# Kernel optimization log

Hardware: AMD Instinct MI355X
Metric: run time of the kernel (lower is better)

## Reference

```python
import jax, jax.numpy as jnp
import numpy as np

B, H, N = 2, 4, 8192
K = 32       # sub_size
TEMP = 2.0   # temperature for the soft permutation indicator


def setup_inputs() -> dict:
    key = jax.random.key(0)
    ranking = jax.random.normal(key, (B, H, N, 1), dtype=jnp.float32)
    return {"ranking": ranking, "i": 0, "j": N}


@jax.custom_vjp
def hsigmoid(x):
    # Hard step indicator (x > 0) with straight-through gradient (CoCN Hsigmoid)
    return (x > 0).astype(x.dtype)

def _hs_fwd(x):
    return hsigmoid(x), None

def _hs_bwd(res, g):
    return (g,)

hsigmoid.defvjp(_hs_fwd, _hs_bwd)


def _windows(x, n, k):
    # circular pad last dim by k-1, then unfold into sliding windows of size k
    xp = jnp.concatenate([x, x[..., :k - 1]], axis=-1)
    idx = jnp.arange(n)[:, None] + jnp.arange(k)[None, :]   # (n, k)
    return xp[..., idx]                                      # (..., n, k)


def reference(ranking, i, j):
    b, h, n = ranking.shape[:3]
    k = K
    r = ranking[..., 0]                                      # (b,h,n)
    order = jnp.argsort(r, axis=2, stable=True)              # (b,h,n) stable sort indices
    r_sorted = jnp.take_along_axis(r, order, axis=2)

    val_win = _windows(r_sorted, n, k)                       # (b,h,n,k)
    idx_win = _windows(order.astype(jnp.float32), n, k).astype(jnp.int32)

    # scatter windows back to original node order == gather by inverse permutation
    inv = jnp.argsort(order, axis=2)                         # (b,h,n)
    val_win = jnp.take_along_axis(val_win, inv[..., None], axis=2)
    idx_win = jnp.take_along_axis(idx_win, inv[..., None], axis=2)

    # within each window, sort by original node index (stable), reorder values alike
    k_order = jnp.argsort(idx_win, axis=-1, stable=True)
    sorted_idx = jnp.take_along_axis(idx_win, k_order, axis=-1)
    val_win = jnp.take_along_axis(val_win, k_order, axis=-1)

    # slice node window [i, i+j)
    val_win = val_win[:, :, i:i + j]                         # (b,h,j,k)
    sorted_idx = sorted_idx[:, :, i:i + j]

    # (b,j,h,k) -> (b*j, h, k, 1)
    x = jnp.transpose(val_win, (0, 2, 1, 3)).reshape(-1, h, k, 1)
    rel = x - jnp.swapaxes(x, -1, -2)                        # (b*j,h,k,k)
    tie_bias = jnp.triu((rel == 0).astype(jnp.float32), 1)   # break ties above diagonal
    rel = rel + tie_bias
    uni = hsigmoid(jax.nn.relu(rel))                         # 1 where strictly greater
    rank = jnp.sum(uni, axis=-2, keepdims=True)              # (b*j,h,1,k)

    ind = jnp.arange(k, dtype=jnp.float32)[:, None] - rank   # (b*j,h,k,k)
    ind = jnp.where(ind < 0, ind + k, ind)
    perm = jnp.exp(-ind * TEMP)
    return perm, sorted_idx
```

## Files before the change

### kernel.cpp

```cpp
#include <hip/hip_runtime.h>
#include <stdint.h>

#define B_ 2
#define H_ 4
#define N_ 8192
#define K_ 32
#define ROWS 8
#define NTOT (ROWS * N_)
#define PERM_ELEMS ((size_t)B_ * N_ * H_ * K_ * K_)

#define JT 1024
#define EPT 8

__device__ __forceinline__ uint32_t mono(float f) {
    uint32_t u = __float_as_uint(f);
    return (u & 0x80000000u) ? ~u : (u | 0x80000000u);
}

__global__ __launch_bounds__(256) void rank_count(const float* __restrict__ ranking,
                                                  int* __restrict__ partial) {
    __shared__ uint64_t jk[JT];
    const int blk = blockIdx.x;
    const int jt  = blk & 7;
    const int it  = (blk >> 3) & 3;
    const int row = blk >> 5;
    const float* rr = ranking + (size_t)row * N_;

    for (int j = threadIdx.x; j < JT; j += 256) {
        const int jj = jt * JT + j;
        jk[j] = ((uint64_t)mono(rr[jj]) << 13) | (uint32_t)jj;
    }

    uint64_t my[EPT];
    const int ibase = it * (EPT * 256) + threadIdx.x;
    #pragma unroll
    for (int e = 0; e < EPT; ++e) {
        const int ii = ibase + e * 256;
        my[e] = ((uint64_t)mono(rr[ii]) << 13) | (uint32_t)ii;
    }
    __syncthreads();

    int cnt[EPT] = {0, 0, 0, 0, 0, 0, 0, 0};
    const ulonglong2* jv = (const ulonglong2*)jk;
    for (int j = 0; j < JT / 2; j += 2) {
        const ulonglong2 a = jv[j];
        const ulonglong2 b = jv[j + 1];
        #pragma unroll
        for (int e = 0; e < EPT; ++e) {
            cnt[e] += (a.x < my[e]);
            cnt[e] += (a.y < my[e]);
            cnt[e] += (b.x < my[e]);
            cnt[e] += (b.y < my[e]);
        }
    }
    #pragma unroll
    for (int e = 0; e < EPT; ++e)
        partial[(size_t)jt * NTOT + (size_t)row * N_ + ibase + e * 256] = cnt[e];
}

__global__ __launch_bounds__(256) void scatter_sorted(const float* __restrict__ ranking,
                                                      const int* __restrict__ partial,
                                                      int2* __restrict__ vid,
                                                      int* __restrict__ inv) {
    const int g = blockIdx.x * 256 + threadIdx.x;
    const int row = g >> 13;
    int s = 0;
    #pragma unroll
    for (int jt = 0; jt < 8; ++jt) s += partial[(size_t)jt * NTOT + g];
    inv[g] = s;
    vid[(size_t)row * N_ + s] = make_int2(__float_as_int(ranking[g]), g & (N_ - 1));
}

__global__ __launch_bounds__(256) void windows_kernel(
    const int2* __restrict__ vid,
    const int* __restrict__ inv,
    float* __restrict__ perm_out,
    float* __restrict__ idx_out)
{
    __shared__ uint64_t wk[8][K_];
    __shared__ float4 cinfo[8][K_];

    const int tid  = threadIdx.x;
    const int wave = tid >> 6;
    const int lane = tid & 63;
    const int half = lane >> 5;
    const int m    = lane & 31;
    const int ws   = wave * 2 + half;

    const int w   = blockIdx.x * 8 + ws;
    const int row = w >> 13;
    const int n   = w & (N_ - 1);

    const int t = inv[(size_t)row * N_ + n];
    int g = t + m; if (g >= N_) g -= N_;
    const int2 vi = vid[(size_t)row * N_ + g];
    const int id = vi.y;
    const int rid = (N_ - 1) - id;
    const uint64_t key2 = ((uint64_t)mono(__int_as_float(vi.x)) << 13) | (uint32_t)rid;

    wk[ws][m] = key2;
    __syncthreads();

    int rank = 0, pos = 0;
    #pragma unroll
    for (int p = 0; p < K_; ++p) {
        const uint64_t kp = wk[ws][p];
        rank += (kp > key2);
        pos  += ((int)((uint32_t)kp & (uint32_t)(N_ - 1)) > rid);
    }

    cinfo[ws][pos] = make_float4(__expf(2.0f * (float)rank),
                                 __int_as_float(rank), (float)id, 0.0f);
    __syncthreads();

    idx_out[((size_t)row * N_ + n) * K_ + m] = cinfo[ws][m].z;

    const int b = row >> 2;
    const int h = row & 3;
    float4* pout = (float4*)(perm_out + (((size_t)b * N_ + n) * H_ + h) * (K_ * K_));

    const int j0 = (m & 7) * 4;
    const float4 c0 = cinfo[ws][j0 + 0];
    const float4 c1 = cinfo[ws][j0 + 1];
    const float4 c2 = cinfo[ws][j0 + 2];
    const float4 c3 = cinfo[ws][j0 + 3];
    const int r0 = __float_as_int(c0.y), r1 = __float_as_int(c1.y);
    const int r2 = __float_as_int(c2.y), r3 = __float_as_int(c3.y);

    const int mbase = m >> 3;
    float a = (mbase & 1 ? 0.13533528f : 1.0f) * (mbase & 2 ? 0.018315639f : 1.0f);
    const float EM8 = 3.3546262e-4f;
    const float E64C = 1.6038108e-28f;
    int mm = mbase;

    #pragma unroll
    for (int q = 0; q < 8; ++q) {
        float4 val;
        val.x = a * c0.x * (mm < r0 ? E64C : 1.0f);
        val.y = a * c1.x * (mm < r1 ? E64C : 1.0f);
        val.z = a * c2.x * (mm < r2 ? E64C : 1.0f);
        val.w = a * c3.x * (mm < r3 ? E64C : 1.0f);
        pout[q * 32 + m] = val;
        a *= EM8;
        mm += 4;
    }
}

extern "C" void kernel_launch(void* const* d_in, const int* in_sizes, int n_in,
                              void* d_out, int out_size, void* d_ws, size_t ws_size,
                              hipStream_t stream) {
    const float* ranking = (const float*)d_in[0];

    char* ws = (char*)d_ws;
    int*  partial = (int*)ws;
    int2* vid     = (int2*)(ws + 2048 * 1024);
    int*  inv     = (int*)(ws + 2560 * 1024);

    float* perm_out = (float*)d_out;
    float* idx_out  = perm_out + PERM_ELEMS;

    hipLaunchKernelGGL(rank_count, dim3(256), dim3(256), 0, stream,
                       ranking, partial);
    hipLaunchKernelGGL(scatter_sorted, dim3(NTOT / 256), dim3(256), 0, stream,
                       ranking, partial, vid, inv);
    hipLaunchKernelGGL(windows_kernel, dim3((ROWS * N_) / 8), dim3(256), 0, stream,
                       vid, inv, perm_out, idx_out);
}
```

Before: 323.3 us.

## Split rank counting into more blocks and iterate windows in sorted order

The rank-count kernel now uses 512-wide j tiles and 4 elements per thread, so it launches 1024 blocks instead of 256 and fills more compute units, with 16 partial sums per element instead of 8. The windows kernel now walks sorted positions directly. Each block loads a 96-entry slice of the sorted array into shared memory once and processes 64 windows across 8 iterations, which removes the inverse-permutation buffer and its per-window global gathers. The trade-off is fewer, longer blocks for the write-heavy windows stage, extra barriers per iteration, and more partial reads in the scatter stage.

Result: faster. 312.7 us (-3.3%).

```diff
diff --git a/kernel.cpp b/kernel.cpp
--- a/kernel.cpp
+++ b/kernel.cpp
@@ -9,8 +9,9 @@
 #define NTOT (ROWS * N_)
 #define PERM_ELEMS ((size_t)B_ * N_ * H_ * K_ * K_)
 
-#define JT 1024
-#define EPT 8
+#define JT 512
+#define EPT 4
+#define NJT 16
 
 __device__ __forceinline__ uint32_t mono(float f) {
     uint32_t u = __float_as_uint(f);
@@ -21,9 +22,9 @@
                                                   int* __restrict__ partial) {
     __shared__ uint64_t jk[JT];
     const int blk = blockIdx.x;
-    const int jt  = blk & 7;
-    const int it  = (blk >> 3) & 3;
-    const int row = blk >> 5;
+    const int jt  = blk & 15;
+    const int it  = (blk >> 4) & 7;
+    const int row = blk >> 7;
     const float* rr = ranking + (size_t)row * N_;
 
     for (int j = threadIdx.x; j < JT; j += 256) {
@@ -40,7 +41,7 @@
     }
     __syncthreads();
 
-    int cnt[EPT] = {0, 0, 0, 0, 0, 0, 0, 0};
+    int cnt[EPT] = {0, 0, 0, 0};
     const ulonglong2* jv = (const ulonglong2*)jk;
     for (int j = 0; j < JT / 2; j += 2) {
         const ulonglong2 a = jv[j];
@@ -60,89 +61,97 @@
 
 __global__ __launch_bounds__(256) void scatter_sorted(const float* __restrict__ ranking,
                                                       const int* __restrict__ partial,
-                                                      int2* __restrict__ vid,
-                                                      int* __restrict__ inv) {
+                                                      int2* __restrict__ vid) {
     const int g = blockIdx.x * 256 + threadIdx.x;
     const int row = g >> 13;
     int s = 0;
     #pragma unroll
-    for (int jt = 0; jt < 8; ++jt) s += partial[(size_t)jt * NTOT + g];
-    inv[g] = s;
+    for (int jt = 0; jt < NJT; ++jt) s += partial[(size_t)jt * NTOT + g];
     vid[(size_t)row * N_ + s] = make_int2(__float_as_int(ranking[g]), g & (N_ - 1));
 }
 
 __global__ __launch_bounds__(256) void windows_kernel(
     const int2* __restrict__ vid,
-    const int* __restrict__ inv,
     float* __restrict__ perm_out,
     float* __restrict__ idx_out)
 {
+    __shared__ int2 vt[96];
     __shared__ uint64_t wk[8][K_];
     __shared__ float4 cinfo[8][K_];
 
-    const int tid  = threadIdx.x;
+    const int tid = threadIdx.x;
+    const int row = blockIdx.x >> 7;
+    const int t0  = (blockIdx.x & 127) * 64;
+
+    for (int q = tid; q < 96; q += 256) {
+        int sidx = t0 + q; if (sidx >= N_) sidx -= N_;
+        vt[q] = vid[(size_t)row * N_ + sidx];
+    }
+    __syncthreads();
+
     const int wave = tid >> 6;
     const int lane = tid & 63;
     const int half = lane >> 5;
     const int m    = lane & 31;
     const int ws   = wave * 2 + half;
+    const int b    = row >> 2;
+    const int h    = row & 3;
 
-    const int w   = blockIdx.x * 8 + ws;
-    const int row = w >> 13;
-    const int n   = w & (N_ - 1);
+    for (int iter = 0; iter < 8; ++iter) {
+        const int q = iter * 8 + ws;
+        const int2 vi = vt[q + m];
+        const int n  = vt[q].y;
+        const int id = vi.y;
+        const int rid = (N_ - 1) - id;
+        const uint64_t key2 =
+            ((uint64_t)mono(__int_as_float(vi.x)) << 13) | (uint32_t)rid;
 
-    const int t = inv[(size_t)row * N_ + n];
-    int g = t + m; if (g >= N_) g -= N_;
-    const int2 vi = vid[(size_t)row * N_ + g];
-    const int id = vi.y;
-    const int rid = (N_ - 1) - id;
-    const uint64_t key2 = ((uint64_t)mono(__int_as_float(vi.x)) << 13) | (uint32_t)rid;
+        wk[ws][m] = key2;
+        __syncthreads();
 
-    wk[ws][m] = key2;
-    __syncthreads();
+        int rank = 0, pos = 0;
+        #pragma unroll
+        for (int p = 0; p < K_; ++p) {
+            const uint64_t kp = wk[ws][p];
+            rank += (kp > key2);
+            pos  += ((int)((uint32_t)kp & (uint32_t)(N_ - 1)) > rid);
+        }
 
-    int rank = 0, pos = 0;
-    #pragma unroll
-    for (int p = 0; p < K_; ++p) {
-        const uint64_t kp = wk[ws][p];
-        rank += (kp > key2);
-        pos  += ((int)((uint32_t)kp & (uint32_t)(N_ - 1)) > rid);
-    }
+        cinfo[ws][pos] = make_float4(__expf(2.0f * (float)rank),
+                                     __int_as_float(rank), (float)id, 0.0f);
+        __syncthreads();
 
-    cinfo[ws][pos] = make_float4(__expf(2.0f * (float)rank),
-                                 __int_as_float(rank), (float)id, 0.0f);
-    __syncthreads();
+        idx_out[((size_t)row * N_ + n) * K_ + m] = cinfo[ws][m].z;
 
-    idx_out[((size_t)row * N_ + n) * K_ + m] = cinfo[ws][m].z;
+        float4* pout =
+            (float4*)(perm_out + (((size_t)b * N_ + n) * H_ + h) * (K_ * K_));
+        const int j0 = (m & 7) * 4;
+        const float4 c0 = cinfo[ws][j0 + 0];
+        const float4 c1 = cinfo[ws][j0 + 1];
+        const float4 c2 = cinfo[ws][j0 + 2];
+        const float4 c3 = cinfo[ws][j0 + 3];
+        const int r0 = __float_as_int(c0.y), r1 = __float_as_int(c1.y);
+        const int r2 = __float_as_int(c2.y), r3 = __float_as_int(c3.y);
 
-    const int b = row >> 2;
-    const int h = row & 3;
-    float4* pout = (float4*)(perm_out + (((size_t)b * N_ + n) * H_ + h) * (K_ * K_));
+        const int mbase = m >> 3;
+        float a = (mbase & 1 ? 0.13533528f : 1.0f) *
+                  (mbase & 2 ? 0.018315639f : 1.0f);
+        const float EM8 = 3.3546262e-4f;
+        const float E64C = 1.6038108e-28f;
+        int mm = mbase;
 
-    const int j0 = (m & 7) * 4;
-    const float4 c0 = cinfo[ws][j0 + 0];
-    const float4 c1 = cinfo[ws][j0 + 1];
-    const float4 c2 = cinfo[ws][j0 + 2];
-    const float4 c3 = cinfo[ws][j0 + 3];
-    const int r0 = __float_as_int(c0.y), r1 = __float_as_int(c1.y);
-    const int r2 = __float_as_int(c2.y), r3 = __float_as_int(c3.y);
-
-    const int mbase = m >> 3;
-    float a = (mbase & 1 ? 0.13533528f : 1.0f) * (mbase & 2 ? 0.018315639f : 1.0f);
-    const float EM8 = 3.3546262e-4f;
-    const float E64C = 1.6038108e-28f;
-    int mm = mbase;
-
-    #pragma unroll
-    for (int q = 0; q < 8; ++q) {
-        float4 val;
-        val.x = a * c0.x * (mm < r0 ? E64C : 1.0f);
-        val.y = a * c1.x * (mm < r1 ? E64C : 1.0f);
-        val.z = a * c2.x * (mm < r2 ? E64C : 1.0f);
-        val.w = a * c3.x * (mm < r3 ? E64C : 1.0f);
-        pout[q * 32 + m] = val;
-        a *= EM8;
-        mm += 4;
+        #pragma unroll
+        for (int qq = 0; qq < 8; ++qq) {
+            float4 val;
+            val.x = a * c0.x * (mm < r0 ? E64C : 1.0f);
+            val.y = a * c1.x * (mm < r1 ? E64C : 1.0f);
+            val.z = a * c2.x * (mm < r2 ? E64C : 1.0f);
+            val.w = a * c3.x * (mm < r3 ? E64C : 1.0f);
+            pout[qq * 32 + m] = val;
+            a *= EM8;
+            mm += 4;
+        }
+        __syncthreads();
     }
 }
 
@@ -153,16 +162,15 @@
 
     char* ws = (char*)d_ws;
     int*  partial = (int*)ws;
-    int2* vid     = (int2*)(ws + 2048 * 1024);
-    int*  inv     = (int*)(ws + 2560 * 1024);
+    int2* vid     = (int2*)(ws + 4 * 1024 * 1024);
 
     float* perm_out = (float*)d_out;
     float* idx_out  = perm_out + PERM_ELEMS;
 
-    hipLaunchKernelGGL(rank_count, dim3(256), dim3(256), 0, stream,
+    hipLaunchKernelGGL(rank_count, dim3(1024), dim3(256), 0, stream,
                        ranking, partial);
     hipLaunchKernelGGL(scatter_sorted, dim3(NTOT / 256), dim3(256), 0, stream,
-                       ranking, partial, vid, inv);
-    hipLaunchKernelGGL(windows_kernel, dim3((ROWS * N_) / 8), dim3(256), 0, stream,
-                       vid, inv, perm_out, idx_out);
+                       ranking, partial, vid);
+    hipLaunchKernelGGL(windows_kernel, dim3(1024), dim3(256), 0, stream,
+                       vid, perm_out, idx_out);
 }
```
